# Kernel optimization log

Hardware: AMD Instinct MI355X
Metric: run time of the kernel (lower is better)

Reference implementation:

```python
import jax, jax.numpy as jnp
import numpy as np

B, NQ, NK, D, H = 4, 1024, 1024, 1024, 16
HD = D // H
SCALE = HD ** -0.5
LN_EPS = 1e-5


def setup_inputs() -> dict:
    key = jax.random.key(0)
    ks = jax.random.split(key, 16)
    s = 0.02
    inp = {
        "query": jax.random.normal(ks[0], (B, NQ, D), jnp.float32),
        "key": jax.random.normal(ks[1], (B, NK, D), jnp.float32),
        "value": jax.random.normal(ks[2], (B, NK, D), jnp.float32),
        # attention projections (torch Linear: [out, in] weights)
        "wq": jax.random.normal(ks[3], (D, D), jnp.float32) * s,
        "bq": jnp.zeros((D,), jnp.float32),
        "wk": jax.random.normal(ks[4], (D, D), jnp.float32) * s,
        "bk": jnp.zeros((D,), jnp.float32),
        "wv": jax.random.normal(ks[5], (D, D), jnp.float32) * s,
        "bv": jnp.zeros((D,), jnp.float32),
        "wo": jax.random.normal(ks[6], (D, D), jnp.float32) * s,
        "bo": jnp.zeros((D,), jnp.float32),
        # vad_proj: Linear(D, D//2) -> GELU -> Linear(D//2, 3) -> Tanh
        "w1": jax.random.normal(ks[7], (D // 2, D), jnp.float32) * s,
        "b1": jnp.zeros((D // 2,), jnp.float32),
        "w2": jax.random.normal(ks[8], (3, D // 2), jnp.float32) * s,
        "b2": jnp.zeros((3,), jnp.float32),
        "vad_lambda": jnp.asarray(0.1, jnp.float32),
        "ln_g": jnp.ones((D,), jnp.float32),
        "ln_b": jnp.zeros((D,), jnp.float32),
    }
    return inp


def _vad(x, w1, b1, w2, b2):
    h = jax.nn.gelu(x @ w1.T + b1, approximate=False)
    return jnp.tanh(h @ w2.T + b2)  # [B, N, 3]


def _layer_norm(x, g, b):
    mu = jnp.mean(x, axis=-1, keepdims=True)
    var = jnp.mean(jnp.square(x - mu), axis=-1, keepdims=True)
    return (x - mu) * jax.lax.rsqrt(var + LN_EPS) * g + b


def reference(query, key, value, wq, bq, wk, bk, wv, bv, wo, bo,
              w1, b1, w2, b2, vad_lambda, ln_g, ln_b):
    Bq, Nq, Dm = query.shape
    Nk = key.shape[1]
    # project and split heads: [B, H, N, HD]
    Q = (query @ wq.T + bq).reshape(Bq, Nq, H, HD).transpose(0, 2, 1, 3)
    K = (key @ wk.T + bk).reshape(Bq, Nk, H, HD).transpose(0, 2, 1, 3)
    V = (value @ wv.T + bv).reshape(Bq, Nk, H, HD).transpose(0, 2, 1, 3)
    scores = jnp.einsum("bhqd,bhkd->bhqk", Q, K) * SCALE  # [B,H,Nq,Nk]
    # VAD affinity: -||v_q[i] - v_k[j]||_2
    vq = _vad(query, w1, b1, w2, b2)  # [B,Nq,3]
    vk = _vad(key, w1, b1, w2, b2)    # [B,Nk,3]
    diff = vq[:, :, None, :] - vk[:, None, :, :]         # [B,Nq,Nk,3]
    affinity = -jnp.sqrt(jnp.sum(diff * diff, axis=-1))  # [B,Nq,Nk]
    guided = scores + vad_lambda * affinity[:, None, :, :]
    attn = jax.nn.softmax(guided, axis=-1)
    out = jnp.einsum("bhqk,bhkd->bhqd", attn, V)
    out = out.transpose(0, 2, 1, 3).reshape(Bq, Nq, Dm)
    out = out @ wo.T + bo
    return _layer_norm(query + out, ln_g, ln_b)
```

## Files before the change

### kernel.cpp

```cpp
#include <hip/hip_runtime.h>
#include <hip/hip_bf16.h>

typedef float f32x4 __attribute__((ext_vector_type(4)));
typedef float f32x16 __attribute__((ext_vector_type(16)));
typedef __bf16 bf16x8 __attribute__((ext_vector_type(8)));
typedef unsigned short us8 __attribute__((ext_vector_type(8)));
typedef unsigned short us4 __attribute__((ext_vector_type(4)));

#define DEVI __device__ __forceinline__
#define LOG2E 1.44269504088896f

DEVI unsigned short f2bf(float x) {
  return __builtin_bit_cast(unsigned short, __float2bfloat16(x));
}
DEVI float bf2f(unsigned short u) {
  return __builtin_bit_cast(float, ((unsigned int)u) << 16);
}
DEVI bf16x8 ldb8(const unsigned short* p) {
  return __builtin_bit_cast(bf16x8, *(const us8*)p);
}
DEVI void gload16(const unsigned short* g, unsigned short* l) {
  __builtin_amdgcn_global_load_lds(
      (const __attribute__((address_space(1))) unsigned int*)(const void*)g,
      (__attribute__((address_space(3))) unsigned int*)(void*)l, 16, 0, 0);
}

__global__ __launch_bounds__(256) void cvt3_k(const float* __restrict__ p0, const float* __restrict__ p1,
                                              const float* __restrict__ p2,
                                              unsigned short* __restrict__ o0, unsigned short* __restrict__ o1,
                                              unsigned short* __restrict__ o2, int n) {
  const float* in;
  unsigned short* out;
  switch (blockIdx.y) {
    case 0: in = p0; out = o0; break;
    case 1: in = p1; out = o1; break;
    default: in = p2; out = o2; break;
  }
  int i = (blockIdx.x * 256 + threadIdx.x) * 8;
  if (i >= n) return;
  float4 a = *(const float4*)(in + i);
  float4 b = *(const float4*)(in + i + 4);
  us8 r = {f2bf(a.x), f2bf(a.y), f2bf(a.z), f2bf(a.w), f2bf(b.x), f2bf(b.y), f2bf(b.z), f2bf(b.w)};
  *(us8*)(out + i) = r;
}

__global__ __launch_bounds__(256) void cvt5_k(const float* __restrict__ p0, const float* __restrict__ p1,
                                              const float* __restrict__ p2, const float* __restrict__ p3,
                                              const float* __restrict__ p4,
                                              unsigned short* __restrict__ o0, unsigned short* __restrict__ o1,
                                              unsigned short* __restrict__ o2, unsigned short* __restrict__ o3,
                                              unsigned short* __restrict__ o4) {
  const float* in;
  unsigned short* out;
  int n = 1048576;
  switch (blockIdx.y) {
    case 0: in = p0; out = o0; break;
    case 1: in = p1; out = o1; break;
    case 2: in = p2; out = o2; break;
    case 3: in = p3; out = o3; break;
    default: in = p4; out = o4; n = 524288; break;
  }
  int i = (blockIdx.x * 256 + threadIdx.x) * 8;
  if (i >= n) return;
  float4 a = *(const float4*)(in + i);
  float4 b = *(const float4*)(in + i + 4);
  us8 r = {f2bf(a.x), f2bf(a.y), f2bf(a.z), f2bf(a.w), f2bf(b.x), f2bf(b.y), f2bf(b.z), f2bf(b.w)};
  *(us8*)(out + i) = r;
}

template <int EPI>
DEVI void gemm_body(const unsigned short* __restrict__ A, const unsigned short* __restrict__ W,
                    const float* __restrict__ bias, void* __restrict__ Cout,
                    int N, int K, int lda, float oscale, int brow, int bcol,
                    unsigned short* As, unsigned short* Bs, int t) {
  const int l = t & 63;
  const int w4 = t >> 6, wr = w4 >> 1, wc = w4 & 1;
  const int l5 = l & 31, hi = l >> 5;
  f32x16 acc[2][2] = {};
  for (int kt = 0; kt < K; kt += 64) {
    __syncthreads();
#pragma unroll
    for (int i = 0; i < 4; ++i) {
      int c = t + i * 256;
      int row = c >> 3, sw = ((c & 7) ^ (row & 7)) * 8;
      gload16(A + (size_t)(brow + row) * lda + kt + sw, As + c * 8);
      gload16(W + (size_t)(bcol + row) * lda + kt + sw, Bs + c * 8);
    }
    __syncthreads();
#pragma unroll
    for (int ks = 0; ks < 4; ++ks) {
      bf16x8 af[2], bfr[2];
      const int ch = (ks * 2 + hi) ^ (l5 & 7);
#pragma unroll
      for (int mi = 0; mi < 2; ++mi)
        af[mi] = ldb8(&As[(wr * 64 + mi * 32 + l5) * 64 + ch * 8]);
#pragma unroll
      for (int ni = 0; ni < 2; ++ni)
        bfr[ni] = ldb8(&Bs[(wc * 64 + ni * 32 + l5) * 64 + ch * 8]);
#pragma unroll
      for (int mi = 0; mi < 2; ++mi)
#pragma unroll
        for (int ni = 0; ni < 2; ++ni)
          acc[mi][ni] = __builtin_amdgcn_mfma_f32_32x32x16_bf16(af[mi], bfr[ni], acc[mi][ni], 0, 0, 0);
    }
  }
#pragma unroll
  for (int mi = 0; mi < 2; ++mi)
#pragma unroll
    for (int ni = 0; ni < 2; ++ni) {
      int col = bcol + wc * 64 + ni * 32 + l5;
      int rowBase = brow + wr * 64 + mi * 32 + hi * 4;
      float bc = (EPI == 3) ? 0.f : bias[col];
#pragma unroll
      for (int reg = 0; reg < 16; ++reg) {
        int row = rowBase + (reg & 3) + 8 * (reg >> 2);
        float v;
        if (EPI == 3)
          v = (acc[mi][ni][reg] + bias[row]) * oscale;
        else if (EPI == 2)
          v = acc[mi][ni][reg] + 0.5f * bc;
        else
          v = (acc[mi][ni][reg] + bc) * oscale;
        if (EPI == 1) v = 0.5f * v * (1.0f + erff(v * 0.70710678118f));
        if (EPI == 2)
          ((float*)Cout)[(size_t)row * N + col] = v;
        else
          ((unsigned short*)Cout)[(size_t)row * N + col] = f2bf(v);
      }
    }
}

__global__ __launch_bounds__(256) void proj_k(const unsigned short* __restrict__ qb, const unsigned short* __restrict__ kb,
                                              const unsigned short* __restrict__ vb,
                                              const unsigned short* __restrict__ wqb, const unsigned short* __restrict__ wkb,
                                              const unsigned short* __restrict__ wvb, const unsigned short* __restrict__ w1b,
                                              const float* __restrict__ bq, const float* __restrict__ bk,
                                              const float* __restrict__ bv, const float* __restrict__ b1,
                                              unsigned short* __restrict__ Qp, unsigned short* __restrict__ Kp,
                                              unsigned short* __restrict__ Vt,
                                              unsigned short* __restrict__ h1q, unsigned short* __restrict__ h1k) {
  __shared__ unsigned short As[8192];
  __shared__ unsigned short Bs[8192];
  const int t = threadIdx.x;
  const int lin = blockIdx.x;
  const int nl = (lin & 7) * 128 + (lin >> 3);
  if (nl < 256) {
    gemm_body<0>(qb, wqb, bq, Qp, 1024, 1024, 1024, 0.125f * LOG2E,
                 (nl >> 3) * 128, (nl & 7) * 128, As, Bs, t);
  } else if (nl < 512) {
    int s = nl - 256;
    gemm_body<0>(kb, wkb, bk, Kp, 1024, 1024, 1024, 1.f,
                 (s >> 3) * 128, (s & 7) * 128, As, Bs, t);
  } else if (nl < 768) {
    int s = nl - 512;
    gemm_body<3>(wvb, vb, bv, Vt, 4096, 1024, 1024, 1.f,
                 (s >> 5) * 128, (s & 31) * 128, As, Bs, t);
  } else {
    int s = nl - 768;
    const unsigned short* A = (s >= 128) ? kb : qb;
    unsigned short* C = (s >= 128) ? h1k : h1q;
    int s2 = s & 127;
    gemm_body<1>(A, w1b, b1, C, 512, 1024, 1024, 1.f,
                 (s2 >> 2) * 128, (s2 & 3) * 128, As, Bs, t);
  }
}

__global__ __launch_bounds__(256) void wo_k(const unsigned short* __restrict__ Obuf, const unsigned short* __restrict__ wob,
                                            const float* __restrict__ bo,
                                            float* __restrict__ tmpA, float* __restrict__ tmpB) {
  __shared__ unsigned short As[8192];
  __shared__ unsigned short Bs[8192];
  const int t = threadIdx.x;
  const int lin = blockIdx.x;
  const int nl = (lin & 7) * 64 + (lin >> 3);
  const int z = nl >> 8, s = nl & 255;
  gemm_body<2>(Obuf + z * 512, wob + z * 512, bo, z ? tmpB : tmpA,
               1024, 512, 1024, 1.f, (s >> 3) * 128, (s & 7) * 128, As, Bs, t);
}

__global__ __launch_bounds__(256) void vad2_k(const unsigned short* __restrict__ h1a, const unsigned short* __restrict__ h1b,
                                              const float* __restrict__ w2, const float* __restrict__ b2,
                                              float* __restrict__ outa, float* __restrict__ outb) {
  const unsigned short* h1 = blockIdx.y ? h1b : h1a;
  float* out = blockIdx.y ? outb : outa;
  const int t = threadIdx.x, l = t & 63, w = t >> 6;
  const int row = blockIdx.x * 4 + w;
  us8 hv = *(const us8*)(h1 + (size_t)row * 512 + l * 8);
  float hf[8];
#pragma unroll
  for (int j = 0; j < 8; ++j) hf[j] = bf2f(hv[j]);
  float s[3];
#pragma unroll
  for (int c = 0; c < 3; ++c) {
    const float* wp = w2 + c * 512 + l * 8;
    float a = 0.f;
#pragma unroll
    for (int j = 0; j < 8; ++j) a += hf[j] * wp[j];
    s[c] = a;
  }
#pragma unroll
  for (int m = 1; m < 64; m <<= 1) {
#pragma unroll
    for (int c = 0; c < 3; ++c) s[c] += __shfl_xor(s[c], m, 64);
  }
  if (l == 0) {
#pragma unroll
    for (int c = 0; c < 3; ++c) out[(size_t)row * 3 + c] = tanhf(s[c] + b2[c]);
  }
}

__global__ __launch_bounds__(256) void aff_k(const float* __restrict__ vq, const float* __restrict__ vk,
                                             const float* __restrict__ plam, unsigned short* __restrict__ aff) {
  __shared__ float vqs[64][3], vks[64][3];
  const int t = threadIdx.x;
  const int b = blockIdx.z, q0 = blockIdx.y * 64, k0 = blockIdx.x * 64;
  const float lam2 = plam[0] * LOG2E;
  if (t < 192) {
    ((float*)vqs)[t] = vq[((size_t)b * 1024 + q0) * 3 + t];
    ((float*)vks)[t] = vk[((size_t)b * 1024 + k0) * 3 + t];
  }
  __syncthreads();
  const int q = t >> 2, kc = (t & 3) * 16;
  const float a0 = vqs[q][0], a1 = vqs[q][1], a2 = vqs[q][2];
  unsigned short o[16];
#pragma unroll
  for (int j = 0; j < 16; ++j) {
    int k = kc + j;
    float dx = a0 - vks[k][0], dy = a1 - vks[k][1], dz = a2 - vks[k][2];
    o[j] = f2bf(-lam2 * sqrtf(dx * dx + dy * dy + dz * dz));
  }
  unsigned short* dst = aff + ((size_t)(b * 1024 + q0 + q)) * 1024 + k0 + kc;
  *(us8*)dst = *(us8*)&o[0];
  *(us8*)(dst + 8) = *(us8*)&o[8];
}

__global__ __launch_bounds__(512, 2) void attn_k(const unsigned short* __restrict__ Qp,
                                                 const unsigned short* __restrict__ Kp,
                                                 const unsigned short* __restrict__ Vt,
                                                 const unsigned short* __restrict__ aff,
                                                 unsigned short* __restrict__ Obuf) {
  __shared__ unsigned short Ks[2][4096];
  __shared__ unsigned short Vs[2][4096];
  __shared__ unsigned short Ps[8][1024];
  const int lin = blockIdx.x + 8 * (blockIdx.y + 16 * blockIdx.z);
  const int nl = (lin & 7) * 64 + (lin >> 3);
  const int qb = nl & 7, h = (nl >> 3) & 15, b = nl >> 7;
  const int t = threadIdx.x, l = t & 63, w = t >> 6;
  const int l4 = l & 15, lg = l >> 4;
  const size_t qrow0 = (size_t)b * 1024 + qb * 128;
  const int hoff = h * 64;

  bf16x8 qf[2];
#pragma unroll
  for (int ks = 0; ks < 2; ++ks)
    qf[ks] = ldb8(Qp + (qrow0 + w * 16 + l4) * 1024 + hoff + ks * 32 + lg * 8);

  {
    const unsigned short* gk = Kp + ((size_t)b * 1024) * 1024 + hoff;
    const unsigned short* gv = Vt + (size_t)hoff * 4096 + (size_t)b * 1024;
    int c = t, row = c >> 3, sw = ((c & 7) ^ (row & 7)) * 8;
    gload16(gk + (size_t)row * 1024 + sw, Ks[0] + c * 8);
    gload16(gv + (size_t)row * 4096 + sw, Vs[0] + c * 8);
  }
  float l_run = 0.f;
  f32x4 accO[4] = {};
  const unsigned short* ab = aff + (qrow0 + w * 16 + l4) * 1024 + lg * 4;
  __syncthreads();

  int cur = 0;
  for (int kt = 0; kt < 16; ++kt) {
    if (kt < 15) {
      const unsigned short* gk = Kp + ((size_t)b * 1024 + (kt + 1) * 64) * 1024 + hoff;
      const unsigned short* gv = Vt + (size_t)hoff * 4096 + (size_t)b * 1024 + (kt + 1) * 64;
      int c = t, row = c >> 3, sw = ((c & 7) ^ (row & 7)) * 8;
      gload16(gk + (size_t)row * 1024 + sw, Ks[cur ^ 1] + c * 8);
      gload16(gv + (size_t)row * 4096 + sw, Vs[cur ^ 1] + c * 8);
    }
    f32x4 sc[4];
#pragma unroll
    for (int jt = 0; jt < 4; ++jt) {
      us4 av = *(const us4*)(ab + kt * 64 + jt * 16);
#pragma unroll
      for (int r = 0; r < 4; ++r) sc[jt][r] = bf2f(av[r]);
    }
    __builtin_amdgcn_s_setprio(1);
#pragma unroll
    for (int jt = 0; jt < 4; ++jt) {
#pragma unroll
      for (int ks = 0; ks < 2; ++ks) {
        bf16x8 kf = ldb8(&Ks[cur][(jt * 16 + l4) * 64 + (((ks * 4 + lg) ^ (l4 & 7))) * 8]);
        sc[jt] = __builtin_amdgcn_mfma_f32_16x16x32_bf16(kf, qf[ks], sc[jt], 0, 0, 0);
      }
    }
    __builtin_amdgcn_s_setprio(0);
    float pv[4][4];
    float rs = 0.f;
#pragma unroll
    for (int jt = 0; jt < 4; ++jt)
#pragma unroll
      for (int r = 0; r < 4; ++r) { pv[jt][r] = exp2f(sc[jt][r]); rs += pv[jt][r]; }
    l_run += rs;
    char* pw = (char*)&Ps[w][0];
#pragma unroll
    for (int jt = 0; jt < 4; ++jt) {
      unsigned int p0, p1;
      asm("v_cvt_pk_bf16_f32 %0, %1, %2" : "=v"(p0) : "v"(pv[jt][0]), "v"(pv[jt][1]));
      asm("v_cvt_pk_bf16_f32 %0, %1, %2" : "=v"(p1) : "v"(pv[jt][2]), "v"(pv[jt][3]));
      int chunk = (jt * 2 + (lg >> 1)) ^ (l4 & 7);
      *(unsigned long long*)(pw + l4 * 128 + chunk * 16 + (lg & 1) * 8) =
          (unsigned long long)p0 | ((unsigned long long)p1 << 32);
    }
    __builtin_amdgcn_s_setprio(1);
#pragma unroll
    for (int js = 0; js < 2; ++js) {
      bf16x8 pa = ldb8(&Ps[w][l4 * 64 + (((js * 4 + lg) ^ (l4 & 7))) * 8]);
#pragma unroll
      for (int dt = 0; dt < 4; ++dt) {
        bf16x8 vf = ldb8(&Vs[cur][(dt * 16 + l4) * 64 + (((js * 4 + lg) ^ (l4 & 7))) * 8]);
        accO[dt] = __builtin_amdgcn_mfma_f32_16x16x32_bf16(pa, vf, accO[dt], 0, 0, 0);
      }
    }
    __builtin_amdgcn_s_setprio(0);
    __syncthreads();
    cur ^= 1;
  }
  l_run += __shfl_xor(l_run, 16, 64);
  l_run += __shfl_xor(l_run, 32, 64);
  float linv = 1.f / l_run;
  float lr[4];
#pragma unroll
  for (int r = 0; r < 4; ++r) lr[r] = __shfl(linv, lg * 4 + r, 16);
#pragma unroll
  for (int dt = 0; dt < 4; ++dt)
#pragma unroll
    for (int r = 0; r < 4; ++r) {
      float v = accO[dt][r] * lr[r];
      Obuf[(qrow0 + w * 16 + lg * 4 + r) * 1024 + hoff + dt * 16 + l4] = f2bf(v);
    }
}

__global__ __launch_bounds__(256) void ln_k(const float* __restrict__ q,
                                            const float* __restrict__ ta,
                                            const float* __restrict__ tb,
                                            const float* __restrict__ g,
                                            const float* __restrict__ bb,
                                            float* __restrict__ out) {
  __shared__ float red[8];
  const int row = blockIdx.x, t = threadIdx.x;
  const int l = t & 63, w = t >> 6;
  const size_t base = (size_t)row * 1024 + t * 4;
  float4 a = *(const float4*)(q + base);
  float4 c = *(const float4*)(ta + base);
  float4 d = *(const float4*)(tb + base);
  float x0 = a.x + c.x + d.x, x1 = a.y + c.y + d.y, x2 = a.z + c.z + d.z, x3 = a.w + c.w + d.w;
  float s = x0 + x1 + x2 + x3;
#pragma unroll
  for (int m = 1; m < 64; m <<= 1) s += __shfl_xor(s, m, 64);
  if (l == 0) red[w] = s;
  __syncthreads();
  float mean = (red[0] + red[1] + red[2] + red[3]) * (1.f / 1024.f);
  float d0 = x0 - mean, d1 = x1 - mean, d2 = x2 - mean, d3 = x3 - mean;
  float v = d0 * d0 + d1 * d1 + d2 * d2 + d3 * d3;
#pragma unroll
  for (int m = 1; m < 64; m <<= 1) v += __shfl_xor(v, m, 64);
  if (l == 0) red[4 + w] = v;
  __syncthreads();
  float var = (red[4] + red[5] + red[6] + red[7]) * (1.f / 1024.f);
  float rstd = rsqrtf(var + 1e-5f);
  float4 gv = *(const float4*)(g + t * 4);
  float4 bv = *(const float4*)(bb + t * 4);
  float4 o;
  o.x = d0 * rstd * gv.x + bv.x;
  o.y = d1 * rstd * gv.y + bv.y;
  o.z = d2 * rstd * gv.z + bv.z;
  o.w = d3 * rstd * gv.w + bv.w;
  *(float4*)(out + (size_t)row * 1024 + t * 4) = o;
}

extern "C" void kernel_launch(void* const* d_in, const int* in_sizes, int n_in,
                              void* d_out, int out_size, void* d_ws, size_t ws_size,
                              hipStream_t stream) {
  const float* query = (const float*)d_in[0];
  const float* key_  = (const float*)d_in[1];
  const float* value = (const float*)d_in[2];
  const float* wq = (const float*)d_in[3];
  const float* bq = (const float*)d_in[4];
  const float* wk = (const float*)d_in[5];
  const float* bk = (const float*)d_in[6];
  const float* wv = (const float*)d_in[7];
  const float* bv = (const float*)d_in[8];
  const float* wo = (const float*)d_in[9];
  const float* bo = (const float*)d_in[10];
  const float* w1 = (const float*)d_in[11];
  const float* b1 = (const float*)d_in[12];
  const float* w2 = (const float*)d_in[13];
  const float* b2 = (const float*)d_in[14];
  const float* lam = (const float*)d_in[15];
  const float* lng = (const float*)d_in[16];
  const float* lnb = (const float*)d_in[17];

  char* ws = (char*)d_ws;
  size_t off = 0;
  auto alloc = [&](size_t n) { char* p = ws + off; off += (n + 255) & ~(size_t)255; return p; };
  unsigned short* qb  = (unsigned short*)alloc(8388608);
  unsigned short* kb  = (unsigned short*)alloc(8388608);
  unsigned short* vb  = (unsigned short*)alloc(8388608);
  unsigned short* wqb = (unsigned short*)alloc(2097152);
  unsigned short* wkb = (unsigned short*)alloc(2097152);
  unsigned short* wvb = (unsigned short*)alloc(2097152);
  unsigned short* wob = (unsigned short*)alloc(2097152);
  unsigned short* w1b = (unsigned short*)alloc(1048576);
  unsigned short* Qp  = (unsigned short*)alloc(8388608);
  unsigned short* Kp  = (unsigned short*)alloc(8388608);
  unsigned short* Vt  = (unsigned short*)alloc(8388608);
  unsigned short* h1q = (unsigned short*)alloc(4194304);
  unsigned short* h1k = (unsigned short*)alloc(4194304);
  float* vadq = (float*)alloc(49152);
  float* vadk = (float*)alloc(49152);
  unsigned short* Obuf = (unsigned short*)alloc(8388608);
  unsigned short* aff = vb;
  float* tmpA = (float*)qb;
  float* tmpB = (float*)Qp;

  cvt3_k<<<dim3(2048, 3), 256, 0, stream>>>(query, key_, value, qb, kb, vb, 4194304);
  cvt5_k<<<dim3(512, 5), 256, 0, stream>>>(wq, wk, wv, wo, w1, wqb, wkb, wvb, wob, w1b);

  proj_k<<<1024, 256, 0, stream>>>(qb, kb, vb, wqb, wkb, wvb, w1b,
                                   bq, bk, bv, b1, Qp, Kp, Vt, h1q, h1k);
  vad2_k<<<dim3(1024, 2), 256, 0, stream>>>(h1q, h1k, w2, b2, vadq, vadk);
  aff_k<<<dim3(16, 16, 4), 256, 0, stream>>>(vadq, vadk, lam, aff);
  attn_k<<<dim3(8, 16, 4), 512, 0, stream>>>(Qp, Kp, Vt, aff, Obuf);
  wo_k<<<512, 256, 0, stream>>>(Obuf, wob, bo, tmpA, tmpB);
  ln_k<<<4096, 256, 0, stream>>>(query, tmpA, tmpB, lng, lnb, (float*)d_out);
}
```

Baseline: 161.0 us.

## Double-buffer GEMM LDS tiles with K-step 32 and prefetch next tile

```diff
diff --git a/kernel.cpp b/kernel.cpp
--- a/kernel.cpp
+++ b/kernel.cpp
@@ -76,33 +76,52 @@
   const int l = t & 63;
   const int w4 = t >> 6, wr = w4 >> 1, wc = w4 & 1;
   const int l5 = l & 31, hi = l >> 5;
+  const int c0 = t, c1 = t + 256;
+  const int r0 = c0 >> 2, r1 = c1 >> 2;
+  const int s0 = ((c0 & 3) ^ ((r0 >> 1) & 3)) * 8;
+  const int s1 = ((c1 & 3) ^ ((r1 >> 1) & 3)) * 8;
+  const unsigned short* Ar0 = A + (size_t)(brow + r0) * lda + s0;
+  const unsigned short* Ar1 = A + (size_t)(brow + r1) * lda + s1;
+  const unsigned short* Wr0 = W + (size_t)(bcol + r0) * lda + s0;
+  const unsigned short* Wr1 = W + (size_t)(bcol + r1) * lda + s1;
   f32x16 acc[2][2] = {};
-  for (int kt = 0; kt < K; kt += 64) {
-    __syncthreads();
-#pragma unroll
-    for (int i = 0; i < 4; ++i) {
-      int c = t + i * 256;
-      int row = c >> 3, sw = ((c & 7) ^ (row & 7)) * 8;
-      gload16(A + (size_t)(brow + row) * lda + kt + sw, As + c * 8);
-      gload16(W + (size_t)(bcol + row) * lda + kt + sw, Bs + c * 8);
-    }
-    __syncthreads();
-#pragma unroll
-    for (int ks = 0; ks < 4; ++ks) {
+  const int nt = K >> 5;
+  gload16(Ar0, As + c0 * 8);
+  gload16(Ar1, As + c1 * 8);
+  gload16(Wr0, Bs + c0 * 8);
+  gload16(Wr1, Bs + c1 * 8);
+  asm volatile("s_waitcnt vmcnt(0)" ::: "memory");
+  __builtin_amdgcn_s_barrier();
+  int cur = 0;
+  for (int kt = 0; kt < nt; ++kt) {
+    if (kt + 1 < nt) {
+      const int ko = (kt + 1) * 32;
+      const int nb = (cur ^ 1) * 4096;
+      gload16(Ar0 + ko, As + nb + c0 * 8);
+      gload16(Ar1 + ko, As + nb + c1 * 8);
+      gload16(Wr0 + ko, Bs + nb + c0 * 8);
+      gload16(Wr1 + ko, Bs + nb + c1 * 8);
+    }
+    const int cb = cur * 4096;
+#pragma unroll
+    for (int ks = 0; ks < 2; ++ks) {
       bf16x8 af[2], bfr[2];
-      const int ch = (ks * 2 + hi) ^ (l5 & 7);
+      const int ch = (((ks * 2 + hi) ^ ((l5 >> 1) & 3))) * 8;
 #pragma unroll
       for (int mi = 0; mi < 2; ++mi)
-        af[mi] = ldb8(&As[(wr * 64 + mi * 32 + l5) * 64 + ch * 8]);
+        af[mi] = ldb8(&As[cb + (wr * 64 + mi * 32 + l5) * 32 + ch]);
 #pragma unroll
       for (int ni = 0; ni < 2; ++ni)
-        bfr[ni] = ldb8(&Bs[(wc * 64 + ni * 32 + l5) * 64 + ch * 8]);
+        bfr[ni] = ldb8(&Bs[cb + (wc * 64 + ni * 32 + l5) * 32 + ch]);
 #pragma unroll
       for (int mi = 0; mi < 2; ++mi)
 #pragma unroll
         for (int ni = 0; ni < 2; ++ni)
           acc[mi][ni] = __builtin_amdgcn_mfma_f32_32x32x16_bf16(af[mi], bfr[ni], acc[mi][ni], 0, 0, 0);
     }
+    asm volatile("s_waitcnt vmcnt(0)" ::: "memory");
+    __builtin_amdgcn_s_barrier();
+    cur ^= 1;
   }
 #pragma unroll
   for (int mi = 0; mi < 2; ++mi)
```

New measurement: 165.4 us. +2.8%, slower.
